# Kernel optimization log

Measured on AMD Instinct MI355X. Metric: run time of the kernel, lower is better.

## Reference

```python
import jax, jax.numpy as jnp
import numpy as np

D_MODEL = 1024
NHEAD = 16
D_K = D_MODEL // NHEAD


def sparsemax(z):
    # sparsemax along last axis (Martins & Astudillo 2016)
    n = z.shape[-1]
    z_sorted = jnp.flip(jnp.sort(z, axis=-1), axis=-1)          # descending
    k = jnp.arange(1, n + 1, dtype=z.dtype)
    z_cumsum = jnp.cumsum(z_sorted, axis=-1)
    support = (1.0 + k * z_sorted) > z_cumsum                    # [..., n] bool
    k_max = jnp.sum(support, axis=-1, keepdims=True)             # [..., 1] int
    tau_sum = jnp.take_along_axis(z_cumsum, k_max - 1, axis=-1)
    tau = (tau_sum - 1.0) / k_max.astype(z.dtype)
    return jnp.maximum(z - tau, 0.0)


def setup_inputs() -> dict:
    key = jax.random.key(0)
    ks = jax.random.split(key, 12)
    B, S = 2, 2048
    s = 1.0 / np.sqrt(D_MODEL)
    inp = {
        'query': jax.random.normal(ks[0], (B, S, D_MODEL), jnp.float32),
        'key':   jax.random.normal(ks[1], (B, S, D_MODEL), jnp.float32),
        'value': jax.random.normal(ks[2], (B, S, D_MODEL), jnp.float32),
        'Wq': jax.random.uniform(ks[3], (D_MODEL, D_MODEL), jnp.float32, -s, s),
        'bq': jax.random.uniform(ks[4], (D_MODEL,), jnp.float32, -s, s),
        'Wk': jax.random.uniform(ks[5], (D_MODEL, D_MODEL), jnp.float32, -s, s),
        'bk': jax.random.uniform(ks[6], (D_MODEL,), jnp.float32, -s, s),
        'Wv': jax.random.uniform(ks[7], (D_MODEL, D_MODEL), jnp.float32, -s, s),
        'bv': jax.random.uniform(ks[8], (D_MODEL,), jnp.float32, -s, s),
        'Wfc': jax.random.uniform(ks[9], (D_MODEL, D_MODEL), jnp.float32, -s, s),
        'bfc': jax.random.uniform(ks[10], (D_MODEL,), jnp.float32, -s, s),
    }
    return inp


def reference(query, key, value, Wq, bq, Wk, bk, Wv, bv, Wfc, bfc):
    B, S, _ = query.shape
    # projections (torch Linear: x @ W.T + b)
    q = (query @ Wq.T + bq).reshape(B, S, NHEAD, D_K).transpose(0, 2, 1, 3)
    k = (key   @ Wk.T + bk).reshape(B, S, NHEAD, D_K).transpose(0, 2, 1, 3)
    v = (value @ Wv.T + bv).reshape(B, S, NHEAD, D_K).transpose(0, 2, 1, 3)
    # scaled dot-product with sparsemax
    logits = jnp.einsum('bhqd,bhkd->bhqk', q, k) / np.sqrt(D_K).astype(jnp.float32)
    attention = sparsemax(logits)                                # [B,H,S,S]
    attn_out = jnp.einsum('bhqk,bhkd->bhqd', attention, v)
    attn_out = attn_out.transpose(0, 2, 1, 3).reshape(B, S, D_MODEL)
    output = attn_out @ Wfc.T + bfc                              # dropout = identity (eval)
    return output, attention
```

## Files before the change

### kernel.cpp

```cpp
#include <hip/hip_runtime.h>
#include <hip/hip_bf16.h>
#include <cstdint>

#define S_LEN  2048
#define DMODEL 1024
#define NHEAD  16
#define M_ROWS 4096
#define HEAD_ELEMS (2048u * 64u)

typedef __attribute__((ext_vector_type(8))) short bf16x8;
typedef __attribute__((ext_vector_type(4))) float f32x4;

__device__ __forceinline__ unsigned short f2bf(float f) {
    __hip_bfloat16 h = __float2bfloat16(f);
    return __builtin_bit_cast(unsigned short, h);
}
__device__ __forceinline__ float bf2f(unsigned short u) {
    return __builtin_bit_cast(float, (unsigned)u << 16);
}

__device__ __forceinline__ float wave_sum64(float v) {
    v += __shfl_xor(v, 32, 64); v += __shfl_xor(v, 16, 64);
    v += __shfl_xor(v, 8, 64);  v += __shfl_xor(v, 4, 64);
    v += __shfl_xor(v, 2, 64);  v += __shfl_xor(v, 1, 64);
    return v;
}
__device__ __forceinline__ float wave_max64(float v) {
    v = fmaxf(v, __shfl_xor(v, 32, 64)); v = fmaxf(v, __shfl_xor(v, 16, 64));
    v = fmaxf(v, __shfl_xor(v, 8, 64));  v = fmaxf(v, __shfl_xor(v, 4, 64));
    v = fmaxf(v, __shfl_xor(v, 2, 64));  v = fmaxf(v, __shfl_xor(v, 1, 64));
    return v;
}
__device__ __forceinline__ int lanes_below(unsigned long long m) {
    return __builtin_amdgcn_mbcnt_hi((unsigned)(m >> 32),
           __builtin_amdgcn_mbcnt_lo((unsigned)m, 0));
}

__global__ __launch_bounds__(256)
void cast_kernel(const float* __restrict__ xq, const float* __restrict__ xk,
                 const float* __restrict__ xv, const float* __restrict__ Wq,
                 const float* __restrict__ Wk, const float* __restrict__ Wv,
                 const float* __restrict__ Wfc, unsigned short* __restrict__ out) {
    const size_t e = ((size_t)blockIdx.x * 256 + threadIdx.x) * 4;
    const size_t M1 = 1u << 20, M4 = 4u << 20;
    const float* src; size_t off;
    if      (e < M4)        { src = xq;  off = e; }
    else if (e < 2 * M4)    { src = xk;  off = e - M4; }
    else if (e < 3 * M4)    { src = xv;  off = e - 2 * M4; }
    else if (e < 13 * M1)   { src = Wq;  off = e - 3 * M4; }
    else if (e < 14 * M1)   { src = Wk;  off = e - 13 * M1; }
    else if (e < 15 * M1)   { src = Wv;  off = e - 14 * M1; }
    else                    { src = Wfc; off = e - 15 * M1; }
    float4 v = *(const float4*)(src + off);
    unsigned int lo = ((unsigned)f2bf(v.y) << 16) | f2bf(v.x);
    unsigned int hi = ((unsigned)f2bf(v.w) << 16) | f2bf(v.z);
    uint2 st = { lo, hi };
    *(uint2*)(out + e) = st;
}

__global__ __launch_bounds__(256)
void qkv_gemm(const unsigned short* __restrict__ x_bf,
              const unsigned short* __restrict__ W_bf,
              const float* __restrict__ bq, const float* __restrict__ bk,
              const float* __restrict__ bv,
              unsigned short* __restrict__ Q_bf, unsigned short* __restrict__ K_bf,
              unsigned short* __restrict__ V_bf) {
    const int which = blockIdx.z;
    const unsigned short* A = x_bf + (size_t)which * (4u << 20);
    const unsigned short* W = W_bf + (size_t)which * (1u << 20);
    const float* bias = (which == 0) ? bq : (which == 1) ? bk : bv;
    unsigned short* dst = (which == 0) ? Q_bf : (which == 1) ? K_bf : V_bf;

    const int row0 = blockIdx.x * 128;
    const int col0 = blockIdx.y * 128;

    __shared__ unsigned short As[128 * 40];
    __shared__ unsigned short Bs[128 * 40];

    const int t = threadIdx.x;
    const int wid = t >> 6, lane = t & 63;
    const int wm = wid >> 1, wn = wid & 1;
    const int l = lane & 15, quad = lane >> 4;

    f32x4 acc[4][4];
#pragma unroll
    for (int i = 0; i < 4; ++i)
#pragma unroll
        for (int j = 0; j < 4; ++j) {
            float b_ = bias[col0 + wn * 64 + j * 16 + l];
            acc[i][j] = (f32x4){ b_, b_, b_, b_ };
        }

    for (int k0 = 0; k0 < DMODEL; k0 += 32) {
        uint4 ar[2], br[2];
#pragma unroll
        for (int i = 0; i < 2; ++i) {
            const int c = t + i * 256, r = c >> 2, q = (c & 3) * 8;
            ar[i] = *(const uint4*)(A + (size_t)(row0 + r) * DMODEL + k0 + q);
            br[i] = *(const uint4*)(W + (size_t)(col0 + r) * DMODEL + k0 + q);
        }
        __syncthreads();
#pragma unroll
        for (int i = 0; i < 2; ++i) {
            const int c = t + i * 256, r = c >> 2, q = (c & 3) * 8;
            *(uint4*)&As[r * 40 + q] = ar[i];
            *(uint4*)&Bs[r * 40 + q] = br[i];
        }
        __syncthreads();
        bf16x8 a[4], b[4];
#pragma unroll
        for (int i = 0; i < 4; ++i)
            a[i] = *(const bf16x8*)&As[(wm * 64 + i * 16 + l) * 40 + quad * 8];
#pragma unroll
        for (int j = 0; j < 4; ++j)
            b[j] = *(const bf16x8*)&Bs[(wn * 64 + j * 16 + l) * 40 + quad * 8];
#pragma unroll
        for (int i = 0; i < 4; ++i)
#pragma unroll
            for (int j = 0; j < 4; ++j)
                acc[i][j] = __builtin_amdgcn_mfma_f32_16x16x32_bf16(a[i], b[j], acc[i][j], 0, 0, 0);
    }

#pragma unroll
    for (int i = 0; i < 4; ++i)
#pragma unroll
        for (int r = 0; r < 4; ++r) {
            const int m = row0 + wm * 64 + i * 16 + quad * 4 + r;
            const int b_ = m >> 11, s = m & 2047;
#pragma unroll
            for (int j = 0; j < 4; ++j) {
                const int n = col0 + wn * 64 + j * 16 + l;
                const int h = n >> 6, d = n & 63;
                dst[(((size_t)(b_ * NHEAD + h)) * S_LEN + s) * 64 + d] = f2bf(acc[i][j][r]);
            }
        }
}

__global__ __launch_bounds__(256)
void logits_gemm(const unsigned short* __restrict__ Q_bf,
                 const unsigned short* __restrict__ K_bf,
                 float* __restrict__ attn) {
    const int bh = blockIdx.z;
    const unsigned short* Qh = Q_bf + (size_t)bh * HEAD_ELEMS;
    const unsigned short* Kh = K_bf + (size_t)bh * HEAD_ELEMS;
    const int row0 = blockIdx.x * 128;
    const int col0 = blockIdx.y * 128;

    __shared__ unsigned short As[128 * 72];
    __shared__ unsigned short Bs[128 * 72];

    const int t = threadIdx.x;
    const int wid = t >> 6, lane = t & 63;
    const int wm = wid >> 1, wn = wid & 1;
    const int l = lane & 15, quad = lane >> 4;

#pragma unroll
    for (int i = 0; i < 4; ++i) {
        const int c = t + i * 256, r = c >> 3, q = (c & 7) * 8;
        *(uint4*)&As[r * 72 + q] = *(const uint4*)(Qh + (size_t)(row0 + r) * 64 + q);
        *(uint4*)&Bs[r * 72 + q] = *(const uint4*)(Kh + (size_t)(col0 + r) * 64 + q);
    }
    __syncthreads();

    f32x4 acc[4][4] = {};
#pragma unroll
    for (int kk = 0; kk < 64; kk += 32) {
        bf16x8 a[4], b[4];
#pragma unroll
        for (int i = 0; i < 4; ++i)
            a[i] = *(const bf16x8*)&As[(wm * 64 + i * 16 + l) * 72 + kk + quad * 8];
#pragma unroll
        for (int j = 0; j < 4; ++j)
            b[j] = *(const bf16x8*)&Bs[(wn * 64 + j * 16 + l) * 72 + kk + quad * 8];
#pragma unroll
        for (int i = 0; i < 4; ++i)
#pragma unroll
            for (int j = 0; j < 4; ++j)
                acc[i][j] = __builtin_amdgcn_mfma_f32_16x16x32_bf16(a[i], b[j], acc[i][j], 0, 0, 0);
    }

    float* ap = attn + (size_t)bh * S_LEN * S_LEN;
#pragma unroll
    for (int i = 0; i < 4; ++i)
#pragma unroll
        for (int r = 0; r < 4; ++r) {
            const int m = row0 + wm * 64 + i * 16 + quad * 4 + r;
#pragma unroll
            for (int j = 0; j < 4; ++j) {
                const int n = col0 + wn * 64 + j * 16 + l;
                ap[(size_t)m * S_LEN + n] = acc[i][j][r] * 0.125f;
            }
        }
}

__global__ __launch_bounds__(256)
void smpv_kernel(float* __restrict__ attn, const unsigned short* __restrict__ V_bf,
                 unsigned short* __restrict__ AO_bf) {
    const int wave = threadIdx.x >> 6;
    const int lane = threadIdx.x & 63;
    const size_t row = (size_t)blockIdx.x * 4 + wave;
    const int bh = (int)(row >> 11), s = (int)(row & 2047);
    const int b_ = bh >> 4, h = bh & 15;
    float4* rp = (float4*)(attn + row * S_LEN);
    const unsigned short* Vh = V_bf + (size_t)bh * HEAD_ELEMS;

    __shared__ uint2 list[4][512];

    float z[32];
#pragma unroll
    for (int r = 0; r < 8; ++r) {
        float4 v = rp[r * 64 + lane];
        z[4 * r + 0] = v.x; z[4 * r + 1] = v.y;
        z[4 * r + 2] = v.z; z[4 * r + 3] = v.w;
    }
    float m = z[0];
#pragma unroll
    for (int j = 1; j < 32; ++j) m = fmaxf(m, z[j]);
    m = wave_max64(m);

    float tau = m - 1.0f;
#pragma unroll 1
    for (int it = 0; it < 8; ++it) {
        float ss = 0.0f, kk = 0.0f;
#pragma unroll
        for (int j = 0; j < 32; ++j)
            if (z[j] > tau) { ss += z[j]; kk += 1.0f; }
        ss = wave_sum64(ss); kk = wave_sum64(kk);
        tau = (ss - 1.0f) / kk;
    }

#pragma unroll
    for (int j = 0; j < 32; ++j) z[j] = fmaxf(z[j] - tau, 0.0f);
#pragma unroll
    for (int r = 0; r < 8; ++r) {
        float4 v = { z[4 * r + 0], z[4 * r + 1], z[4 * r + 2], z[4 * r + 3] };
        rp[r * 64 + lane] = v;
    }

    float acc = 0.0f;
#pragma unroll 1
    for (int rr = 0; rr < 4; ++rr) {
        int base = 0;
#pragma unroll
        for (int e = 0; e < 8; ++e) {
            const int r = rr * 2 + (e >> 2), jj = e & 3;
            const float pv = z[4 * r + jj];
            const unsigned long long mk = __ballot(pv > 0.0f);
            if (pv > 0.0f) {
                const int pos = base + lanes_below(mk);
                uint2 kp = { (unsigned)(r * 256 + lane * 4 + jj),
                             __builtin_bit_cast(unsigned, pv) };
                list[wave][pos] = kp;
            }
            base += __popcll(mk);
        }
        __threadfence_block();
        const int total = base;
        int i = 0;
        for (; i + 2 <= total; i += 2) {
            uint2 kp0 = list[wave][i], kp1 = list[wave][i + 1];
            float v0 = bf2f(Vh[(size_t)kp0.x * 64 + lane]);
            float v1 = bf2f(Vh[(size_t)kp1.x * 64 + lane]);
            acc += __builtin_bit_cast(float, kp0.y) * v0;
            acc += __builtin_bit_cast(float, kp1.y) * v1;
        }
        if (i < total) {
            uint2 kp0 = list[wave][i];
            acc += __builtin_bit_cast(float, kp0.y) * bf2f(Vh[(size_t)kp0.x * 64 + lane]);
        }
        __threadfence_block();
    }

    AO_bf[((size_t)(b_ * S_LEN + s)) * DMODEL + h * 64 + lane] = f2bf(acc);
}

__global__ __launch_bounds__(256)
void fc_gemm(const unsigned short* __restrict__ AO_bf,
             const unsigned short* __restrict__ Wfc_bf,
             const float* __restrict__ bfc, float* __restrict__ out) {
    const int row0 = blockIdx.x * 128;
    const int col0 = blockIdx.y * 128;

    __shared__ unsigned short As[128 * 40];
    __shared__ unsigned short Bs[128 * 40];

    const int t = threadIdx.x;
    const int wid = t >> 6, lane = t & 63;
    const int wm = wid >> 1, wn = wid & 1;
    const int l = lane & 15, quad = lane >> 4;

    f32x4 acc[4][4];
#pragma unroll
    for (int i = 0; i < 4; ++i)
#pragma unroll
        for (int j = 0; j < 4; ++j) {
            float b_ = bfc[col0 + wn * 64 + j * 16 + l];
            acc[i][j] = (f32x4){ b_, b_, b_, b_ };
        }

    for (int k0 = 0; k0 < DMODEL; k0 += 32) {
        uint4 ar[2], br[2];
#pragma unroll
        for (int i = 0; i < 2; ++i) {
            const int c = t + i * 256, r = c >> 2, q = (c & 3) * 8;
            ar[i] = *(const uint4*)(AO_bf + (size_t)(row0 + r) * DMODEL + k0 + q);
            br[i] = *(const uint4*)(Wfc_bf + (size_t)(col0 + r) * DMODEL + k0 + q);
        }
        __syncthreads();
#pragma unroll
        for (int i = 0; i < 2; ++i) {
            const int c = t + i * 256, r = c >> 2, q = (c & 3) * 8;
            *(uint4*)&As[r * 40 + q] = ar[i];
            *(uint4*)&Bs[r * 40 + q] = br[i];
        }
        __syncthreads();
        bf16x8 a[4], b[4];
#pragma unroll
        for (int i = 0; i < 4; ++i)
            a[i] = *(const bf16x8*)&As[(wm * 64 + i * 16 + l) * 40 + quad * 8];
#pragma unroll
        for (int j = 0; j < 4; ++j)
            b[j] = *(const bf16x8*)&Bs[(wn * 64 + j * 16 + l) * 40 + quad * 8];
#pragma unroll
        for (int i = 0; i < 4; ++i)
#pragma unroll
            for (int j = 0; j < 4; ++j)
                acc[i][j] = __builtin_amdgcn_mfma_f32_16x16x32_bf16(a[i], b[j], acc[i][j], 0, 0, 0);
    }

#pragma unroll
    for (int i = 0; i < 4; ++i)
#pragma unroll
        for (int r = 0; r < 4; ++r) {
            const int m = row0 + wm * 64 + i * 16 + quad * 4 + r;
#pragma unroll
            for (int j = 0; j < 4; ++j) {
                const int n = col0 + wn * 64 + j * 16 + l;
                out[(size_t)m * DMODEL + n] = acc[i][j][r];
            }
        }
}

extern "C" void kernel_launch(void* const* d_in, const int* in_sizes, int n_in,
                              void* d_out, int out_size, void* d_ws, size_t ws_size,
                              hipStream_t stream) {
    const float* q   = (const float*)d_in[0];
    const float* k   = (const float*)d_in[1];
    const float* v   = (const float*)d_in[2];
    const float* Wq  = (const float*)d_in[3];
    const float* bq  = (const float*)d_in[4];
    const float* Wk  = (const float*)d_in[5];
    const float* bk  = (const float*)d_in[6];
    const float* Wv  = (const float*)d_in[7];
    const float* bv  = (const float*)d_in[8];
    const float* Wfc = (const float*)d_in[9];
    const float* bfc = (const float*)d_in[10];

    float* out  = (float*)d_out;
    float* attn = out + (size_t)M_ROWS * DMODEL;

    char* ws = (char*)d_ws;
    unsigned short* x_bf = (unsigned short*)ws;
    unsigned short* W_bf = (unsigned short*)(ws + (24u << 20));
    unsigned short* Q_bf = (unsigned short*)(ws + (32u << 20));
    unsigned short* K_bf = (unsigned short*)(ws + (40u << 20));
    unsigned short* V_bf = (unsigned short*)(ws + (48u << 20));
    unsigned short* AO_bf = x_bf;

    cast_kernel<<<16384, 256, 0, stream>>>(q, k, v, Wq, Wk, Wv, Wfc, x_bf);
    qkv_gemm<<<dim3(32, 8, 3), 256, 0, stream>>>(x_bf, W_bf, bq, bk, bv, Q_bf, K_bf, V_bf);
    logits_gemm<<<dim3(16, 16, 32), 256, 0, stream>>>(Q_bf, K_bf, attn);
    smpv_kernel<<<16384, 256, 0, stream>>>(attn, V_bf, AO_bf);
    fc_gemm<<<dim3(32, 8), 256, 0, stream>>>(AO_bf, W_bf + (3u << 20), bfc, out);
}
```

Before: 991.7 us.

## Fuse fp32-to-bf16 cast into GEMM loads and store Q/K/V in row-major layout

Removes the separate cast kernel. The QKV and FC GEMMs now read fp32 inputs and weights directly and convert them to bf16 in registers before staging them in shared memory. The QKV epilogue now goes through shared memory and writes coalesced 16-byte stores into a [B,S,DMODEL] layout instead of scattered per-head 2-byte stores. Downstream kernels index heads with a DMODEL stride. This saves one pass over about 50MB of fp32 data, but doubles the global bytes each GEMM tile loads, and the V gathers in the sparsemax kernel become strided.

```diff
diff --git a/kernel.cpp b/kernel.cpp
--- a/kernel.cpp
+++ b/kernel.cpp
@@ -6,7 +6,6 @@
 #define DMODEL 1024
 #define NHEAD  16
 #define M_ROWS 4096
-#define HEAD_ELEMS (2048u * 64u)
 
 typedef __attribute__((ext_vector_type(8))) short bf16x8;
 typedef __attribute__((ext_vector_type(4))) float f32x4;
@@ -17,6 +16,14 @@
 }
 __device__ __forceinline__ float bf2f(unsigned short u) {
     return __builtin_bit_cast(float, (unsigned)u << 16);
+}
+__device__ __forceinline__ uint4 pack8(float4 a, float4 b) {
+    uint4 u;
+    u.x = ((unsigned)f2bf(a.y) << 16) | f2bf(a.x);
+    u.y = ((unsigned)f2bf(a.w) << 16) | f2bf(a.z);
+    u.z = ((unsigned)f2bf(b.y) << 16) | f2bf(b.x);
+    u.w = ((unsigned)f2bf(b.w) << 16) | f2bf(b.z);
+    return u;
 }
 
 __device__ __forceinline__ float wave_sum64(float v) {
@@ -37,45 +44,26 @@
 }
 
 __global__ __launch_bounds__(256)
-void cast_kernel(const float* __restrict__ xq, const float* __restrict__ xk,
-                 const float* __restrict__ xv, const float* __restrict__ Wq,
-                 const float* __restrict__ Wk, const float* __restrict__ Wv,
-                 const float* __restrict__ Wfc, unsigned short* __restrict__ out) {
-    const size_t e = ((size_t)blockIdx.x * 256 + threadIdx.x) * 4;
-    const size_t M1 = 1u << 20, M4 = 4u << 20;
-    const float* src; size_t off;
-    if      (e < M4)        { src = xq;  off = e; }
-    else if (e < 2 * M4)    { src = xk;  off = e - M4; }
-    else if (e < 3 * M4)    { src = xv;  off = e - 2 * M4; }
-    else if (e < 13 * M1)   { src = Wq;  off = e - 3 * M4; }
-    else if (e < 14 * M1)   { src = Wk;  off = e - 13 * M1; }
-    else if (e < 15 * M1)   { src = Wv;  off = e - 14 * M1; }
-    else                    { src = Wfc; off = e - 15 * M1; }
-    float4 v = *(const float4*)(src + off);
-    unsigned int lo = ((unsigned)f2bf(v.y) << 16) | f2bf(v.x);
-    unsigned int hi = ((unsigned)f2bf(v.w) << 16) | f2bf(v.z);
-    uint2 st = { lo, hi };
-    *(uint2*)(out + e) = st;
-}
-
-__global__ __launch_bounds__(256)
-void qkv_gemm(const unsigned short* __restrict__ x_bf,
-              const unsigned short* __restrict__ W_bf,
+void qkv_gemm(const float* __restrict__ xq, const float* __restrict__ xk,
+              const float* __restrict__ xv,
+              const float* __restrict__ Wq, const float* __restrict__ Wk,
+              const float* __restrict__ Wv,
               const float* __restrict__ bq, const float* __restrict__ bk,
               const float* __restrict__ bv,
               unsigned short* __restrict__ Q_bf, unsigned short* __restrict__ K_bf,
               unsigned short* __restrict__ V_bf) {
     const int which = blockIdx.z;
-    const unsigned short* A = x_bf + (size_t)which * (4u << 20);
-    const unsigned short* W = W_bf + (size_t)which * (1u << 20);
+    const float* A    = (which == 0) ? xq : (which == 1) ? xk : xv;
+    const float* W    = (which == 0) ? Wq : (which == 1) ? Wk : Wv;
     const float* bias = (which == 0) ? bq : (which == 1) ? bk : bv;
     unsigned short* dst = (which == 0) ? Q_bf : (which == 1) ? K_bf : V_bf;
 
     const int row0 = blockIdx.x * 128;
     const int col0 = blockIdx.y * 128;
 
-    __shared__ unsigned short As[128 * 40];
-    __shared__ unsigned short Bs[128 * 40];
+    __shared__ unsigned short SMEM[10240];
+    unsigned short* As = SMEM;
+    unsigned short* Bs = SMEM + 5120;
 
     const int t = threadIdx.x;
     const int wid = t >> 6, lane = t & 63;
@@ -96,8 +84,12 @@
 #pragma unroll
         for (int i = 0; i < 2; ++i) {
             const int c = t + i * 256, r = c >> 2, q = (c & 3) * 8;
-            ar[i] = *(const uint4*)(A + (size_t)(row0 + r) * DMODEL + k0 + q);
-            br[i] = *(const uint4*)(W + (size_t)(col0 + r) * DMODEL + k0 + q);
+            const float* ap = A + (size_t)(row0 + r) * DMODEL + k0 + q;
+            const float* wp = W + (size_t)(col0 + r) * DMODEL + k0 + q;
+            float4 a0 = *(const float4*)ap, a1 = *(const float4*)(ap + 4);
+            float4 w0 = *(const float4*)wp, w1 = *(const float4*)(wp + 4);
+            ar[i] = pack8(a0, a1);
+            br[i] = pack8(w0, w1);
         }
         __syncthreads();
 #pragma unroll
@@ -121,19 +113,30 @@
                 acc[i][j] = __builtin_amdgcn_mfma_f32_16x16x32_bf16(a[i], b[j], acc[i][j], 0, 0, 0);
     }
 
-#pragma unroll
-    for (int i = 0; i < 4; ++i)
-#pragma unroll
-        for (int r = 0; r < 4; ++r) {
-            const int m = row0 + wm * 64 + i * 16 + quad * 4 + r;
-            const int b_ = m >> 11, s = m & 2047;
-#pragma unroll
-            for (int j = 0; j < 4; ++j) {
-                const int n = col0 + wn * 64 + j * 16 + l;
-                const int h = n >> 6, d = n & 63;
-                dst[(((size_t)(b_ * NHEAD + h)) * S_LEN + s) * 64 + d] = f2bf(acc[i][j][r]);
-            }
-        }
+    __syncthreads();
+    unsigned short* Cs = SMEM;
+#pragma unroll 1
+    for (int jh = 0; jh < 2; ++jh) {
+        if (wn == jh) {
+#pragma unroll
+            for (int i = 0; i < 4; ++i)
+#pragma unroll
+                for (int j = 0; j < 4; ++j)
+#pragma unroll
+                    for (int r = 0; r < 4; ++r)
+                        Cs[(wm * 64 + i * 16 + quad * 4 + r) * 72 + j * 16 + l] =
+                            f2bf(acc[i][j][r]);
+        }
+        __syncthreads();
+#pragma unroll
+        for (int it = 0; it < 4; ++it) {
+            const int idx = t + it * 256;
+            const int row = idx >> 3, c8 = (idx & 7) * 8;
+            *(uint4*)(dst + (size_t)(row0 + row) * DMODEL + col0 + jh * 64 + c8) =
+                *(const uint4*)&Cs[row * 72 + c8];
+        }
+        __syncthreads();
+    }
 }
 
 __global__ __launch_bounds__(256)
@@ -141,8 +144,9 @@
                  const unsigned short* __restrict__ K_bf,
                  float* __restrict__ attn) {
     const int bh = blockIdx.z;
-    const unsigned short* Qh = Q_bf + (size_t)bh * HEAD_ELEMS;
-    const unsigned short* Kh = K_bf + (size_t)bh * HEAD_ELEMS;
+    const int b_ = bh >> 4, h = bh & 15;
+    const unsigned short* Qh = Q_bf + ((size_t)b_ * S_LEN) * DMODEL + h * 64;
+    const unsigned short* Kh = K_bf + ((size_t)b_ * S_LEN) * DMODEL + h * 64;
     const int row0 = blockIdx.x * 128;
     const int col0 = blockIdx.y * 128;
 
@@ -157,8 +161,8 @@
 #pragma unroll
     for (int i = 0; i < 4; ++i) {
         const int c = t + i * 256, r = c >> 3, q = (c & 7) * 8;
-        *(uint4*)&As[r * 72 + q] = *(const uint4*)(Qh + (size_t)(row0 + r) * 64 + q);
-        *(uint4*)&Bs[r * 72 + q] = *(const uint4*)(Kh + (size_t)(col0 + r) * 64 + q);
+        *(uint4*)&As[r * 72 + q] = *(const uint4*)(Qh + (size_t)(row0 + r) * DMODEL + q);
+        *(uint4*)&Bs[r * 72 + q] = *(const uint4*)(Kh + (size_t)(col0 + r) * DMODEL + q);
     }
     __syncthreads();
 
@@ -202,7 +206,7 @@
     const int bh = (int)(row >> 11), s = (int)(row & 2047);
     const int b_ = bh >> 4, h = bh & 15;
     float4* rp = (float4*)(attn + row * S_LEN);
-    const unsigned short* Vh = V_bf + (size_t)bh * HEAD_ELEMS;
+    const unsigned short* Vh = V_bf + ((size_t)b_ * S_LEN) * DMODEL + h * 64;
 
     __shared__ uint2 list[4][512];
 
@@ -259,14 +263,14 @@
         int i = 0;
         for (; i + 2 <= total; i += 2) {
             uint2 kp0 = list[wave][i], kp1 = list[wave][i + 1];
-            float v0 = bf2f(Vh[(size_t)kp0.x * 64 + lane]);
-            float v1 = bf2f(Vh[(size_t)kp1.x * 64 + lane]);
+            float v0 = bf2f(Vh[(size_t)kp0.x * DMODEL + lane]);
+            float v1 = bf2f(Vh[(size_t)kp1.x * DMODEL + lane]);
             acc += __builtin_bit_cast(float, kp0.y) * v0;
             acc += __builtin_bit_cast(float, kp1.y) * v1;
         }
         if (i < total) {
             uint2 kp0 = list[wave][i];
-            acc += __builtin_bit_cast(float, kp0.y) * bf2f(Vh[(size_t)kp0.x * 64 + lane]);
+            acc += __builtin_bit_cast(float, kp0.y) * bf2f(Vh[(size_t)kp0.x * DMODEL + lane]);
         }
         __threadfence_block();
     }
@@ -276,7 +280,7 @@
 
 __global__ __launch_bounds__(256)
 void fc_gemm(const unsigned short* __restrict__ AO_bf,
-             const unsigned short* __restrict__ Wfc_bf,
+             const float* __restrict__ Wfc,
              const float* __restrict__ bfc, float* __restrict__ out) {
     const int row0 = blockIdx.x * 128;
     const int col0 = blockIdx.y * 128;
@@ -304,7 +308,9 @@
         for (int i = 0; i < 2; ++i) {
             const int c = t + i * 256, r = c >> 2, q = (c & 3) * 8;
             ar[i] = *(const uint4*)(AO_bf + (size_t)(row0 + r) * DMODEL + k0 + q);
-            br[i] = *(const uint4*)(Wfc_bf + (size_t)(col0 + r) * DMODEL + k0 + q);
+            const float* wp = Wfc + (size_t)(col0 + r) * DMODEL + k0 + q;
+            float4 w0 = *(const float4*)wp, w1 = *(const float4*)(wp + 4);
+            br[i] = pack8(w0, w1);
         }
         __syncthreads();
 #pragma unroll
@@ -360,16 +366,14 @@
     float* attn = out + (size_t)M_ROWS * DMODEL;
 
     char* ws = (char*)d_ws;
-    unsigned short* x_bf = (unsigned short*)ws;
-    unsigned short* W_bf = (unsigned short*)(ws + (24u << 20));
-    unsigned short* Q_bf = (unsigned short*)(ws + (32u << 20));
-    unsigned short* K_bf = (unsigned short*)(ws + (40u << 20));
-    unsigned short* V_bf = (unsigned short*)(ws + (48u << 20));
-    unsigned short* AO_bf = x_bf;
-
-    cast_kernel<<<16384, 256, 0, stream>>>(q, k, v, Wq, Wk, Wv, Wfc, x_bf);
-    qkv_gemm<<<dim3(32, 8, 3), 256, 0, stream>>>(x_bf, W_bf, bq, bk, bv, Q_bf, K_bf, V_bf);
+    unsigned short* Q_bf  = (unsigned short*)ws;
+    unsigned short* K_bf  = (unsigned short*)(ws + (8u << 20));
+    unsigned short* V_bf  = (unsigned short*)(ws + (16u << 20));
+    unsigned short* AO_bf = (unsigned short*)(ws + (24u << 20));
+
+    qkv_gemm<<<dim3(32, 8, 3), 256, 0, stream>>>(q, k, v, Wq, Wk, Wv,
+                                                  bq, bk, bv, Q_bf, K_bf, V_bf);
     logits_gemm<<<dim3(16, 16, 32), 256, 0, stream>>>(Q_bf, K_bf, attn);
     smpv_kernel<<<16384, 256, 0, stream>>>(attn, V_bf, AO_bf);
-    fc_gemm<<<dim3(32, 8), 256, 0, stream>>>(AO_bf, W_bf + (3u << 20), bfc, out);
-}
+    fc_gemm<<<dim3(32, 8), 256, 0, stream>>>(AO_bf, Wfc, bfc, out);
+}
```

New measurement: 907.8 us. 8.5% less time.
